# Optimization experiments

Hardware: AMD Instinct MI355X
Metric: run time of the kernel (lower is better)

## Reference

```python
import jax, jax.numpy as jnp
import numpy as np

DIM = 768
HID = 4 * DIM
NUM_EXPERTS = 8


def setup_inputs() -> dict:
    key = jax.random.key(0)
    ks = jax.random.split(key, 8)
    B, T = 2, 2048
    x = jax.random.normal(ks[0], (B, T, DIM), dtype=jnp.float32)
    mapped_tokens = jax.random.randint(ks[1], (B * T,), 0, NUM_EXPERTS)
    s_in = 1.0 / np.sqrt(DIM)   # nn.Linear init scale for fan_in=DIM
    s_hid = 1.0 / np.sqrt(HID)  # for fan_in=HID
    Wg = jax.random.uniform(ks[2], (NUM_EXPERTS, DIM, HID), jnp.float32, -s_in, s_in)
    bg = jax.random.uniform(ks[3], (NUM_EXPERTS, HID), jnp.float32, -s_in, s_in)
    Wi = jax.random.uniform(ks[4], (NUM_EXPERTS, DIM, HID), jnp.float32, -s_in, s_in)
    bi = jax.random.uniform(ks[5], (NUM_EXPERTS, HID), jnp.float32, -s_in, s_in)
    Wo = jax.random.uniform(ks[6], (NUM_EXPERTS, HID, DIM), jnp.float32, -s_hid, s_hid)
    bo = jax.random.uniform(ks[7], (NUM_EXPERTS, DIM), jnp.float32, -s_hid, s_hid)
    return {"x": x, "mapped_tokens": mapped_tokens, "Wg": Wg, "bg": bg,
            "Wi": Wi, "bi": bi, "Wo": Wo, "bo": bo}


def reference(x, mapped_tokens, Wg, bg, Wi, bi, Wo, bo):
    B, T, C = x.shape
    xf = x.reshape(-1, C)                      # [N, C], N = B*T
    out = jnp.zeros_like(xf)
    E = Wg.shape[0]
    for e in range(E):                         # small fixed expert loop
        h = jax.nn.silu(xf @ Wg[e] + bg[e]) * (xf @ Wi[e] + bi[e])  # [N, 4C]
        y = h @ Wo[e] + bo[e]                  # [N, C]
        out = out + jnp.where((mapped_tokens == e)[:, None], y, 0.0)
    return out.reshape(B, T, C)
```

## Files before the change

### kernel.cpp

```cpp
#include <hip/hip_runtime.h>
#include <hip/hip_bf16.h>
#include <stdint.h>

#define DIM 768
#define HID 3072
#define NE 8
#define NTOK 4096
#define PADROWS 5120
#define MAXT 40

#define M_PO 0
#define M_NTILES 24
#define M_TE 25
#define M_TR 65
#define M_TV 105
#define M_PERM 256
#define XE_OFF (64 * 1024)
#define H_OFF  8126464

typedef short short8 __attribute__((ext_vector_type(8)));
typedef short short4v __attribute__((ext_vector_type(4)));
typedef float f32x4 __attribute__((ext_vector_type(4)));

__device__ __forceinline__ short bfs(float f) {
  __hip_bfloat16 h = __float2bfloat16(f);
  short s; __builtin_memcpy(&s, &h, 2); return s;
}

__global__ void route_kernel(const int* __restrict__ map, int* __restrict__ meta) {
  __shared__ int scnt[NE];
  __shared__ int scur[NE];
  int t = threadIdx.x;
  if (t < NE) scnt[t] = 0;
  __syncthreads();
  for (int i = t; i < NTOK; i += 256) atomicAdd(&scnt[map[i]], 1);
  __syncthreads();
  if (t == 0) {
    int acc = 0, nt = 0;
    for (int e = 0; e < NE; ++e) {
      meta[M_PO + e] = acc;
      scur[e] = acc;
      int c = scnt[e];
      for (int r = 0; r < c; r += 128) {
        meta[M_TE + nt] = e;
        meta[M_TR + nt] = acc + r;
        meta[M_TV + nt] = (c - r < 128) ? (c - r) : 128;
        ++nt;
      }
      acc += (c + 127) & ~127;
    }
    meta[M_PO + 8] = acc;
    meta[M_NTILES] = nt;
  }
  for (int i = t; i < PADROWS; i += 256) meta[M_PERM + i] = 0;
  __syncthreads();
  for (int i = t; i < NTOK; i += 256) {
    int e = map[i];
    int slot = atomicAdd(&scur[e], 1);
    meta[M_PERM + slot] = i;
  }
}

__global__ void gather_kernel(const float* __restrict__ x, const int* __restrict__ meta,
                              short* __restrict__ Xe) {
  int id = blockIdx.x * 256 + threadIdx.x;
  if (id >= PADROWS * 96) return;
  int row = id / 96;
  int sub = id - row * 96;
  int tok = meta[M_PERM + row];
  const float* src = x + (size_t)tok * DIM + sub * 8;
  float4 a = *(const float4*)src;
  float4 b = *(const float4*)(src + 4);
  short8 v;
  v[0] = bfs(a.x); v[1] = bfs(a.y); v[2] = bfs(a.z); v[3] = bfs(a.w);
  v[4] = bfs(b.x); v[5] = bfs(b.y); v[6] = bfs(b.z); v[7] = bfs(b.w);
  int blk = sub >> 3, s = sub & 7;
  int off = row * (DIM * 2) + blk * 128 + ((s * 16) ^ ((row & 7) << 4));
  *(short8*)((char*)Xe + off) = v;
}

__device__ __forceinline__ void write_bt2(char* bt0, char* bt1,
                                          const float4 (&br)[2][4], int kb, int jb) {
  char* bts[2] = {bt0, bt1};
  #pragma unroll
  for (int mat = 0; mat < 2; ++mat) {
    #pragma unroll
    for (int i = 0; i < 4; ++i) {
      int c2 = jb * 4 + i;
      short4v s;
      s[0] = bfs(((const float*)&br[mat][0])[i]);
      s[1] = bfs(((const float*)&br[mat][1])[i]);
      s[2] = bfs(((const float*)&br[mat][2])[i]);
      s[3] = bfs(((const float*)&br[mat][3])[i]);
      *(short4v*)(bts[mat] + c2 * 128 + ((kb * 8) ^ ((c2 & 7) << 4))) = s;
    }
  }
}

__device__ __forceinline__ void write_bt1(char* bt, const float4 (&br)[4], int kb, int jb) {
  #pragma unroll
  for (int i = 0; i < 4; ++i) {
    int c2 = jb * 4 + i;
    short4v s;
    s[0] = bfs(((const float*)&br[0])[i]);
    s[1] = bfs(((const float*)&br[1])[i]);
    s[2] = bfs(((const float*)&br[2])[i]);
    s[3] = bfs(((const float*)&br[3])[i]);
    *(short4v*)(bt + c2 * 128 + ((kb * 8) ^ ((c2 & 7) << 4))) = s;
  }
}

__launch_bounds__(256, 3)
__global__ void gemm1_kernel(const short* __restrict__ Xe, const float* __restrict__ Wg,
                             const float* __restrict__ bg, const float* __restrict__ Wi,
                             const float* __restrict__ bi, const int* __restrict__ meta,
                             short* __restrict__ H) {
  int nt = meta[M_NTILES];
  int ty = blockIdx.y;
  if (ty >= nt) return;
  int e = meta[M_TE + ty], row0 = meta[M_TR + ty], rows = meta[M_TV + ty];
  int j0 = blockIdx.x * 64;
  __shared__ short As[2][128 * 64];
  __shared__ short Bt[2][64 * 64];
  int tid = threadIdx.x;
  int lane = tid & 63, w = tid >> 6;
  int wm = w >> 1, wn = w & 1;
  int kb = tid & 15, jb = tid >> 4;
  const float* W0 = Wg + (size_t)e * DIM * HID;
  const float* W1 = Wi + (size_t)e * DIM * HID;
  f32x4 ag[4][2] = {};
  f32x4 av[4][2] = {};
  float4 br[2][4];

  #pragma unroll
  for (int mat = 0; mat < 2; ++mat) {
    const float* base = (mat ? W1 : W0) + (size_t)(kb * 4) * HID + j0 + jb * 4;
    #pragma unroll
    for (int r = 0; r < 4; ++r) br[mat][r] = *(const float4*)(base + r * HID);
  }
  #pragma unroll
  for (int q = 0; q < 4; ++q) {
    const char* src = (const char*)Xe + (size_t)(row0 + (w * 4 + q) * 8 + (lane >> 3)) * (DIM * 2)
                      + (lane & 7) * 16;
    __builtin_amdgcn_global_load_lds((const __attribute__((address_space(1))) void*)src,
                                     (__attribute__((address_space(3))) void*)((char*)&As[0][0] + (w * 4 + q) * 1024),
                                     16, 0, 0);
  }
  write_bt2((char*)&Bt[0][0], (char*)&Bt[1][0], br, kb, jb);
  __syncthreads();

  int cur = 0;
  for (int kt = 0; kt < 12; ++kt) {
    if (kt < 11) {
      #pragma unroll
      for (int mat = 0; mat < 2; ++mat) {
        const float* base = (mat ? W1 : W0) + (size_t)((kt + 1) * 64 + kb * 4) * HID + j0 + jb * 4;
        #pragma unroll
        for (int r = 0; r < 4; ++r) br[mat][r] = *(const float4*)(base + r * HID);
      }
      #pragma unroll
      for (int q = 0; q < 4; ++q) {
        const char* src = (const char*)Xe + (size_t)(row0 + (w * 4 + q) * 8 + (lane >> 3)) * (DIM * 2)
                          + (kt + 1) * 128 + (lane & 7) * 16;
        __builtin_amdgcn_global_load_lds((const __attribute__((address_space(1))) void*)src,
                                         (__attribute__((address_space(3))) void*)((char*)&As[cur ^ 1][0] + (w * 4 + q) * 1024),
                                         16, 0, 0);
      }
    }
    #pragma unroll
    for (int kf = 0; kf < 2; ++kf) {
      short8 af[4];
      #pragma unroll
      for (int m = 0; m < 4; ++m) {
        int r = wm * 64 + m * 16 + (lane & 15);
        int coff = (kf * 64 + (lane >> 4) * 16) ^ ((r & 7) << 4);
        af[m] = *(const short8*)((const char*)&As[cur][0] + r * 128 + coff);
      }
      #pragma unroll
      for (int n = 0; n < 2; ++n) {
        int c = wn * 32 + n * 16 + (lane & 15);
        int coff = (kf * 64 + (lane >> 4) * 16) ^ ((c & 7) << 4);
        short8 b0 = *(const short8*)((const char*)&Bt[0][0] + c * 128 + coff);
        short8 b1 = *(const short8*)((const char*)&Bt[1][0] + c * 128 + coff);
        #pragma unroll
        for (int m = 0; m < 4; ++m) {
          ag[m][n] = __builtin_amdgcn_mfma_f32_16x16x32_bf16(af[m], b0, ag[m][n], 0, 0, 0);
          av[m][n] = __builtin_amdgcn_mfma_f32_16x16x32_bf16(af[m], b1, av[m][n], 0, 0, 0);
        }
      }
    }
    asm volatile("s_waitcnt lgkmcnt(0)\n\ts_barrier" ::: "memory");
    if (kt < 11) write_bt2((char*)&Bt[0][0], (char*)&Bt[1][0], br, kb, jb);
    __syncthreads();
    cur ^= 1;
  }

  #pragma unroll
  for (int n = 0; n < 2; ++n) {
    int c = j0 + wn * 32 + n * 16 + (lane & 15);
    float bgv = bg[e * HID + c];
    float biv = bi[e * HID + c];
    #pragma unroll
    for (int m = 0; m < 4; ++m) {
      #pragma unroll
      for (int r = 0; r < 4; ++r) {
        int rl = wm * 64 + m * 16 + (lane >> 4) * 4 + r;
        if (rl < rows) {
          float g = ag[m][n][r] + bgv;
          float v = av[m][n][r] + biv;
          float h = g / (1.f + __expf(-g)) * v;
          int grow = row0 + rl;
          int off = grow * (HID * 2) + (c >> 6) * 128 + ((2 * (c & 63)) ^ ((grow & 7) << 4));
          *(short*)((char*)H + off) = bfs(h);
        }
      }
    }
  }
}

__launch_bounds__(256, 3)
__global__ void gemm2_kernel(const short* __restrict__ H, const float* __restrict__ Wo,
                             const float* __restrict__ bo, const int* __restrict__ meta,
                             float* __restrict__ out) {
  int nt = meta[M_NTILES];
  int ty = blockIdx.y;
  if (ty >= nt) return;
  int e = meta[M_TE + ty], row0 = meta[M_TR + ty], rows = meta[M_TV + ty];
  int j0 = blockIdx.x * 64;
  __shared__ short As[2][128 * 64];
  __shared__ short Bt[64 * 64];
  int tid = threadIdx.x;
  int lane = tid & 63, w = tid >> 6;
  int wm = w >> 1, wn = w & 1;
  int kb = tid & 15, jb = tid >> 4;
  const float* W2 = Wo + (size_t)e * HID * DIM;
  f32x4 acc[4][2] = {};
  float4 br[4];

  #pragma unroll
  for (int r = 0; r < 4; ++r)
    br[r] = *(const float4*)(W2 + (size_t)(kb * 4 + r) * DIM + j0 + jb * 4);
  #pragma unroll
  for (int q = 0; q < 4; ++q) {
    const char* src = (const char*)H + (size_t)(row0 + (w * 4 + q) * 8 + (lane >> 3)) * (HID * 2)
                      + (lane & 7) * 16;
    __builtin_amdgcn_global_load_lds((const __attribute__((address_space(1))) void*)src,
                                     (__attribute__((address_space(3))) void*)((char*)&As[0][0] + (w * 4 + q) * 1024),
                                     16, 0, 0);
  }
  write_bt1((char*)&Bt[0], br, kb, jb);
  __syncthreads();

  int cur = 0;
  for (int kt = 0; kt < 48; ++kt) {
    if (kt < 47) {
      #pragma unroll
      for (int r = 0; r < 4; ++r)
        br[r] = *(const float4*)(W2 + (size_t)((kt + 1) * 64 + kb * 4 + r) * DIM + j0 + jb * 4);
      #pragma unroll
      for (int q = 0; q < 4; ++q) {
        const char* src = (const char*)H + (size_t)(row0 + (w * 4 + q) * 8 + (lane >> 3)) * (HID * 2)
                          + (kt + 1) * 128 + (lane & 7) * 16;
        __builtin_amdgcn_global_load_lds((const __attribute__((address_space(1))) void*)src,
                                         (__attribute__((address_space(3))) void*)((char*)&As[cur ^ 1][0] + (w * 4 + q) * 1024),
                                         16, 0, 0);
      }
    }
    #pragma unroll
    for (int kf = 0; kf < 2; ++kf) {
      short8 af[4];
      #pragma unroll
      for (int m = 0; m < 4; ++m) {
        int r = wm * 64 + m * 16 + (lane & 15);
        int coff = (kf * 64 + (lane >> 4) * 16) ^ ((r & 7) << 4);
        af[m] = *(const short8*)((const char*)&As[cur][0] + r * 128 + coff);
      }
      #pragma unroll
      for (int n = 0; n < 2; ++n) {
        int c = wn * 32 + n * 16 + (lane & 15);
        int coff = (kf * 64 + (lane >> 4) * 16) ^ ((c & 7) << 4);
        short8 b0 = *(const short8*)((const char*)&Bt[0] + c * 128 + coff);
        #pragma unroll
        for (int m = 0; m < 4; ++m) {
          acc[m][n] = __builtin_amdgcn_mfma_f32_16x16x32_bf16(af[m], b0, acc[m][n], 0, 0, 0);
        }
      }
    }
    asm volatile("s_waitcnt lgkmcnt(0)\n\ts_barrier" ::: "memory");
    if (kt < 47) write_bt1((char*)&Bt[0], br, kb, jb);
    __syncthreads();
    cur ^= 1;
  }

  #pragma unroll
  for (int n = 0; n < 2; ++n) {
    int c = j0 + wn * 32 + n * 16 + (lane & 15);
    float bov = bo[e * DIM + c];
    #pragma unroll
    for (int m = 0; m < 4; ++m) {
      #pragma unroll
      for (int r = 0; r < 4; ++r) {
        int rl = wm * 64 + m * 16 + (lane >> 4) * 4 + r;
        if (rl < rows) {
          int tok = meta[M_PERM + row0 + rl];
          out[(size_t)tok * DIM + c] = acc[m][n][r] + bov;
        }
      }
    }
  }
}

extern "C" void kernel_launch(void* const* d_in, const int* in_sizes, int n_in,
                              void* d_out, int out_size, void* d_ws, size_t ws_size,
                              hipStream_t stream) {
  (void)in_sizes; (void)n_in; (void)out_size; (void)ws_size;
  const float* x   = (const float*)d_in[0];
  const int*   map = (const int*)d_in[1];
  const float* Wg  = (const float*)d_in[2];
  const float* bg  = (const float*)d_in[3];
  const float* Wi  = (const float*)d_in[4];
  const float* bi  = (const float*)d_in[5];
  const float* Wo  = (const float*)d_in[6];
  const float* bo  = (const float*)d_in[7];
  float* out = (float*)d_out;
  int* meta = (int*)d_ws;
  short* Xe = (short*)((char*)d_ws + XE_OFF);
  short* H  = (short*)((char*)d_ws + H_OFF);

  hipLaunchKernelGGL(route_kernel, dim3(1), dim3(256), 0, stream, map, meta);
  hipLaunchKernelGGL(gather_kernel, dim3(PADROWS * 96 / 256), dim3(256), 0, stream, x, meta, Xe);
  hipLaunchKernelGGL(gemm1_kernel, dim3(HID / 64, MAXT), dim3(256), 0, stream,
                     Xe, Wg, bg, Wi, bi, meta, H);
  hipLaunchKernelGGL(gemm2_kernel, dim3(DIM / 64, MAXT), dim3(256), 0, stream,
                     H, Wo, bo, meta, out);
}
```

Before: 419.4 us.

## Pre-convert expert weights to swizzled bf16 transposed layout before the GEMMs

Adds a prep kernel that converts Wg, Wi and Wo from fp32 to bf16, transposed and swizzled into the workspace, on every call. The new GEMM kernels then fetch both operands directly into LDS with global_load_lds, with no per-tile register conversion, but they drop the double buffering and use single-buffered loads with two barriers per k-step. The cost is an extra full read of the fp32 weights and a bf16 write per call, in exchange for lighter GEMM main loops. The old kernels remain as a fallback when the workspace is too small.

```diff
diff --git a/kernel.cpp b/kernel.cpp
--- a/kernel.cpp
+++ b/kernel.cpp
@@ -16,7 +16,11 @@
 #define M_TV 105
 #define M_PERM 256
 #define XE_OFF (64 * 1024)
-#define H_OFF  8126464
+#define H_OFF  8126464ull
+#define WG_OFF 39583744ull
+#define WI_OFF 77332480ull
+#define WO_OFF 115081216ull
+#define WS_NEED 152829952ull
 
 typedef short short8 __attribute__((ext_vector_type(8)));
 typedef short short4v __attribute__((ext_vector_type(4)));
@@ -79,6 +83,223 @@
   *(short8*)((char*)Xe + off) = v;
 }
 
+__global__ void prep_kernel(const float* __restrict__ src, short* __restrict__ dst,
+                            int K, int N) {
+  __shared__ short lds[64 * 136];
+  int e = blockIdx.z;
+  int n0 = blockIdx.x * 64, k0 = blockIdx.y * 128;
+  const float* s = src + (size_t)e * K * N + (size_t)k0 * N + n0;
+  int t = threadIdx.x;
+  int kk = t >> 3, nn = (t & 7) * 8;
+  #pragma unroll
+  for (int p = 0; p < 4; ++p) {
+    int k = kk + 32 * p;
+    float4 a = *(const float4*)(s + (size_t)k * N + nn);
+    float4 b = *(const float4*)(s + (size_t)k * N + nn + 4);
+    short v0 = bfs(a.x), v1 = bfs(a.y), v2 = bfs(a.z), v3 = bfs(a.w);
+    short v4 = bfs(b.x), v5 = bfs(b.y), v6 = bfs(b.z), v7 = bfs(b.w);
+    lds[(nn + 0) * 136 + k] = v0; lds[(nn + 1) * 136 + k] = v1;
+    lds[(nn + 2) * 136 + k] = v2; lds[(nn + 3) * 136 + k] = v3;
+    lds[(nn + 4) * 136 + k] = v4; lds[(nn + 5) * 136 + k] = v5;
+    lds[(nn + 6) * 136 + k] = v6; lds[(nn + 7) * 136 + k] = v7;
+  }
+  __syncthreads();
+  int n = t & 63, sb = (t >> 6) * 4;
+  int gn = n0 + n;
+  char* drow = (char*)(dst + (size_t)e * N * K) + (size_t)gn * (K * 2);
+  int swz = (gn & 7) << 4;
+  #pragma unroll
+  for (int i = 0; i < 4; ++i) {
+    int sc = sb + i;
+    int kglob = k0 + sc * 8;
+    short8 v = *(const short8*)&lds[n * 136 + sc * 8];
+    *(short8*)(drow + (kglob >> 6) * 128 + ((((kglob & 63) >> 3) * 16) ^ swz)) = v;
+  }
+}
+
+__launch_bounds__(256, 4)
+__global__ void gemm1_kernel(const short* __restrict__ Xe, const short* __restrict__ WgT,
+                             const short* __restrict__ WiT, const float* __restrict__ bg,
+                             const float* __restrict__ bi, const int* __restrict__ meta,
+                             short* __restrict__ H) {
+  int nt = meta[M_NTILES];
+  int ty = blockIdx.y;
+  if (ty >= nt) return;
+  int e = meta[M_TE + ty], row0 = meta[M_TR + ty], rows = meta[M_TV + ty];
+  int j0 = blockIdx.x * 64;
+  __shared__ short As[128 * 64];
+  __shared__ short Bs[128 * 64];
+  int tid = threadIdx.x;
+  int lane = tid & 63, w = tid >> 6;
+  int wm = w >> 1, wn = w & 1;
+  const short* WgTe = WgT + (size_t)e * HID * DIM;
+  const short* WiTe = WiT + (size_t)e * HID * DIM;
+  f32x4 ag[4][2] = {};
+  f32x4 av[4][2] = {};
+
+  const char* aSrc[4];
+  const char* bSrc[4];
+  #pragma unroll
+  for (int q = 0; q < 4; ++q) {
+    int rA = (w * 4 + q) * 8 + (lane >> 3);
+    aSrc[q] = (const char*)Xe + (size_t)(row0 + rA) * (DIM * 2) + (lane & 7) * 16;
+    int rB = (w * 4 + q) * 8 + (lane >> 3);
+    const short* Wt = (rB < 64) ? WgTe : WiTe;
+    bSrc[q] = (const char*)Wt + (size_t)(j0 + (rB & 63)) * (DIM * 2) + (lane & 7) * 16;
+  }
+
+  for (int kt = 0; kt < DIM / 64; ++kt) {
+    #pragma unroll
+    for (int q = 0; q < 4; ++q) {
+      __builtin_amdgcn_global_load_lds((const __attribute__((address_space(1))) void*)aSrc[q],
+                                       (__attribute__((address_space(3))) void*)((char*)As + (w * 4 + q) * 1024),
+                                       16, 0, 0);
+      aSrc[q] += 128;
+    }
+    #pragma unroll
+    for (int q = 0; q < 4; ++q) {
+      __builtin_amdgcn_global_load_lds((const __attribute__((address_space(1))) void*)bSrc[q],
+                                       (__attribute__((address_space(3))) void*)((char*)Bs + (w * 4 + q) * 1024),
+                                       16, 0, 0);
+      bSrc[q] += 128;
+    }
+    __syncthreads();
+    #pragma unroll
+    for (int kf = 0; kf < 2; ++kf) {
+      short8 af[4];
+      #pragma unroll
+      for (int m = 0; m < 4; ++m) {
+        int r = wm * 64 + m * 16 + (lane & 15);
+        int coff = (kf * 64 + (lane >> 4) * 16) ^ ((r & 7) << 4);
+        af[m] = *(const short8*)((const char*)As + r * 128 + coff);
+      }
+      #pragma unroll
+      for (int n = 0; n < 2; ++n) {
+        int c = wn * 32 + n * 16 + (lane & 15);
+        int coff = (kf * 64 + (lane >> 4) * 16) ^ ((c & 7) << 4);
+        short8 b0 = *(const short8*)((const char*)Bs + c * 128 + coff);
+        short8 b1 = *(const short8*)((const char*)Bs + (64 + c) * 128 + coff);
+        #pragma unroll
+        for (int m = 0; m < 4; ++m) {
+          ag[m][n] = __builtin_amdgcn_mfma_f32_16x16x32_bf16(af[m], b0, ag[m][n], 0, 0, 0);
+          av[m][n] = __builtin_amdgcn_mfma_f32_16x16x32_bf16(af[m], b1, av[m][n], 0, 0, 0);
+        }
+      }
+    }
+    __syncthreads();
+  }
+
+  #pragma unroll
+  for (int n = 0; n < 2; ++n) {
+    int c = j0 + wn * 32 + n * 16 + (lane & 15);
+    float bgv = bg[e * HID + c];
+    float biv = bi[e * HID + c];
+    #pragma unroll
+    for (int m = 0; m < 4; ++m) {
+      #pragma unroll
+      for (int r = 0; r < 4; ++r) {
+        int rl = wm * 64 + m * 16 + (lane >> 4) * 4 + r;
+        if (rl < rows) {
+          float g = ag[m][n][r] + bgv;
+          float v = av[m][n][r] + biv;
+          float h = g / (1.f + __expf(-g)) * v;
+          int grow = row0 + rl;
+          int off = grow * (HID * 2) + (c >> 6) * 128 + ((2 * (c & 63)) ^ ((grow & 7) << 4));
+          *(short*)((char*)H + off) = bfs(h);
+        }
+      }
+    }
+  }
+}
+
+__launch_bounds__(256, 4)
+__global__ void gemm2_kernel(const short* __restrict__ H, const short* __restrict__ WoT,
+                             const float* __restrict__ bo, const int* __restrict__ meta,
+                             float* __restrict__ out) {
+  int nt = meta[M_NTILES];
+  int ty = blockIdx.y;
+  if (ty >= nt) return;
+  int j0 = blockIdx.x * 64;
+  if (j0 >= DIM) return;
+  int e = meta[M_TE + ty], row0 = meta[M_TR + ty], rows = meta[M_TV + ty];
+  __shared__ short As[128 * 64];
+  __shared__ short Bs[64 * 64];
+  int tid = threadIdx.x;
+  int lane = tid & 63, w = tid >> 6;
+  int wm = w >> 1, wn = w & 1;
+  const short* WoTe = WoT + (size_t)e * DIM * HID;
+  f32x4 acc[4][2] = {};
+
+  const char* aSrc[4];
+  const char* bSrc[2];
+  #pragma unroll
+  for (int q = 0; q < 4; ++q) {
+    int rA = (w * 4 + q) * 8 + (lane >> 3);
+    aSrc[q] = (const char*)H + (size_t)(row0 + rA) * (HID * 2) + (lane & 7) * 16;
+  }
+  #pragma unroll
+  for (int q = 0; q < 2; ++q) {
+    int rB = (w * 2 + q) * 8 + (lane >> 3);
+    bSrc[q] = (const char*)WoTe + (size_t)(j0 + rB) * (HID * 2) + (lane & 7) * 16;
+  }
+
+  for (int kt = 0; kt < HID / 64; ++kt) {
+    #pragma unroll
+    for (int q = 0; q < 4; ++q) {
+      __builtin_amdgcn_global_load_lds((const __attribute__((address_space(1))) void*)aSrc[q],
+                                       (__attribute__((address_space(3))) void*)((char*)As + (w * 4 + q) * 1024),
+                                       16, 0, 0);
+      aSrc[q] += 128;
+    }
+    #pragma unroll
+    for (int q = 0; q < 2; ++q) {
+      __builtin_amdgcn_global_load_lds((const __attribute__((address_space(1))) void*)bSrc[q],
+                                       (__attribute__((address_space(3))) void*)((char*)Bs + (w * 2 + q) * 1024),
+                                       16, 0, 0);
+      bSrc[q] += 128;
+    }
+    __syncthreads();
+    #pragma unroll
+    for (int kf = 0; kf < 2; ++kf) {
+      short8 af[4];
+      #pragma unroll
+      for (int m = 0; m < 4; ++m) {
+        int r = wm * 64 + m * 16 + (lane & 15);
+        int coff = (kf * 64 + (lane >> 4) * 16) ^ ((r & 7) << 4);
+        af[m] = *(const short8*)((const char*)As + r * 128 + coff);
+      }
+      #pragma unroll
+      for (int n = 0; n < 2; ++n) {
+        int c = wn * 32 + n * 16 + (lane & 15);
+        int coff = (kf * 64 + (lane >> 4) * 16) ^ ((c & 7) << 4);
+        short8 b0 = *(const short8*)((const char*)Bs + c * 128 + coff);
+        #pragma unroll
+        for (int m = 0; m < 4; ++m) {
+          acc[m][n] = __builtin_amdgcn_mfma_f32_16x16x32_bf16(af[m], b0, acc[m][n], 0, 0, 0);
+        }
+      }
+    }
+    __syncthreads();
+  }
+
+  #pragma unroll
+  for (int n = 0; n < 2; ++n) {
+    int c = j0 + wn * 32 + n * 16 + (lane & 15);
+    float bov = bo[e * DIM + c];
+    #pragma unroll
+    for (int m = 0; m < 4; ++m) {
+      #pragma unroll
+      for (int r = 0; r < 4; ++r) {
+        int rl = wm * 64 + m * 16 + (lane >> 4) * 4 + r;
+        if (rl < rows) {
+          int tok = meta[M_PERM + row0 + rl];
+          out[(size_t)tok * DIM + c] = acc[m][n][r] + bov;
+        }
+      }
+    }
+  }
+}
+
 __device__ __forceinline__ void write_bt2(char* bt0, char* bt1,
                                           const float4 (&br)[2][4], int kb, int jb) {
   char* bts[2] = {bt0, bt1};
@@ -111,10 +332,10 @@
 }
 
 __launch_bounds__(256, 3)
-__global__ void gemm1_kernel(const short* __restrict__ Xe, const float* __restrict__ Wg,
-                             const float* __restrict__ bg, const float* __restrict__ Wi,
-                             const float* __restrict__ bi, const int* __restrict__ meta,
-                             short* __restrict__ H) {
+__global__ void gemm1_fb(const short* __restrict__ Xe, const float* __restrict__ Wg,
+                         const float* __restrict__ bg, const float* __restrict__ Wi,
+                         const float* __restrict__ bi, const int* __restrict__ meta,
+                         short* __restrict__ H) {
   int nt = meta[M_NTILES];
   int ty = blockIdx.y;
   if (ty >= nt) return;
@@ -131,7 +352,6 @@
   f32x4 ag[4][2] = {};
   f32x4 av[4][2] = {};
   float4 br[2][4];
-
   #pragma unroll
   for (int mat = 0; mat < 2; ++mat) {
     const float* base = (mat ? W1 : W0) + (size_t)(kb * 4) * HID + j0 + jb * 4;
@@ -148,7 +368,6 @@
   }
   write_bt2((char*)&Bt[0][0], (char*)&Bt[1][0], br, kb, jb);
   __syncthreads();
-
   int cur = 0;
   for (int kt = 0; kt < 12; ++kt) {
     if (kt < 11) {
@@ -194,7 +413,6 @@
     __syncthreads();
     cur ^= 1;
   }
-
   #pragma unroll
   for (int n = 0; n < 2; ++n) {
     int c = j0 + wn * 32 + n * 16 + (lane & 15);
@@ -219,9 +437,9 @@
 }
 
 __launch_bounds__(256, 3)
-__global__ void gemm2_kernel(const short* __restrict__ H, const float* __restrict__ Wo,
-                             const float* __restrict__ bo, const int* __restrict__ meta,
-                             float* __restrict__ out) {
+__global__ void gemm2_fb(const short* __restrict__ H, const float* __restrict__ Wo,
+                         const float* __restrict__ bo, const int* __restrict__ meta,
+                         float* __restrict__ out) {
   int nt = meta[M_NTILES];
   int ty = blockIdx.y;
   if (ty >= nt) return;
@@ -236,7 +454,6 @@
   const float* W2 = Wo + (size_t)e * HID * DIM;
   f32x4 acc[4][2] = {};
   float4 br[4];
-
   #pragma unroll
   for (int r = 0; r < 4; ++r)
     br[r] = *(const float4*)(W2 + (size_t)(kb * 4 + r) * DIM + j0 + jb * 4);
@@ -250,7 +467,6 @@
   }
   write_bt1((char*)&Bt[0], br, kb, jb);
   __syncthreads();
-
   int cur = 0;
   for (int kt = 0; kt < 48; ++kt) {
     if (kt < 47) {
@@ -291,7 +507,6 @@
     __syncthreads();
     cur ^= 1;
   }
-
   #pragma unroll
   for (int n = 0; n < 2; ++n) {
     int c = j0 + wn * 32 + n * 16 + (lane & 15);
@@ -313,7 +528,7 @@
 extern "C" void kernel_launch(void* const* d_in, const int* in_sizes, int n_in,
                               void* d_out, int out_size, void* d_ws, size_t ws_size,
                               hipStream_t stream) {
-  (void)in_sizes; (void)n_in; (void)out_size; (void)ws_size;
+  (void)in_sizes; (void)n_in; (void)out_size;
   const float* x   = (const float*)d_in[0];
   const int*   map = (const int*)d_in[1];
   const float* Wg  = (const float*)d_in[2];
@@ -329,8 +544,22 @@
 
   hipLaunchKernelGGL(route_kernel, dim3(1), dim3(256), 0, stream, map, meta);
   hipLaunchKernelGGL(gather_kernel, dim3(PADROWS * 96 / 256), dim3(256), 0, stream, x, meta, Xe);
-  hipLaunchKernelGGL(gemm1_kernel, dim3(HID / 64, MAXT), dim3(256), 0, stream,
-                     Xe, Wg, bg, Wi, bi, meta, H);
-  hipLaunchKernelGGL(gemm2_kernel, dim3(DIM / 64, MAXT), dim3(256), 0, stream,
-                     H, Wo, bo, meta, out);
-}
+
+  if (ws_size >= WS_NEED) {
+    short* WgT = (short*)((char*)d_ws + WG_OFF);
+    short* WiT = (short*)((char*)d_ws + WI_OFF);
+    short* WoT = (short*)((char*)d_ws + WO_OFF);
+    hipLaunchKernelGGL(prep_kernel, dim3(HID / 64, DIM / 128, NE), dim3(256), 0, stream, Wg, WgT, DIM, HID);
+    hipLaunchKernelGGL(prep_kernel, dim3(HID / 64, DIM / 128, NE), dim3(256), 0, stream, Wi, WiT, DIM, HID);
+    hipLaunchKernelGGL(prep_kernel, dim3(DIM / 64, HID / 128, NE), dim3(256), 0, stream, Wo, WoT, HID, DIM);
+    hipLaunchKernelGGL(gemm1_kernel, dim3(HID / 64, MAXT), dim3(256), 0, stream,
+                       Xe, WgT, WiT, bg, bi, meta, H);
+    hipLaunchKernelGGL(gemm2_kernel, dim3(16, MAXT), dim3(256), 0, stream,
+                       H, WoT, bo, meta, out);
+  } else {
+    hipLaunchKernelGGL(gemm1_fb, dim3(HID / 64, MAXT), dim3(256), 0, stream,
+                       Xe, Wg, bg, Wi, bi, meta, H);
+    hipLaunchKernelGGL(gemm2_fb, dim3(DIM / 64, MAXT), dim3(256), 0, stream,
+                       H, Wo, bo, meta, out);
+  }
+}
```

Measured after the change: 438.3 us. 4.5% more time.
